# Optimization experiments

Hardware: AMD Instinct MI355X
Metric: run time of the kernel (lower is better)

## Reference

```python
import jax, jax.numpy as jnp
import numpy as np
import math

B, D, N, M = 8, 64, 4096, 4096


def setup_inputs() -> dict:
    key = jax.random.key(0)
    k1, k2, k3, k4 = jax.random.split(key, 4)
    return {
        "src_embedding": jax.random.normal(k1, (B, D, N), dtype=jnp.float32),
        "tgt_embedding": jax.random.normal(k2, (B, D, M), dtype=jnp.float32),
        "src": jax.random.normal(k3, (B, 3, N), dtype=jnp.float32),
        "tgt": jax.random.normal(k4, (B, 3, M), dtype=jnp.float32),
    }


def reference(src_embedding, tgt_embedding, src, tgt):
    d_k = src_embedding.shape[1]
    # scores: [B, N, M] = src_emb^T @ tgt_emb / sqrt(d)
    scores = jnp.einsum("bdn,bdm->bnm", src_embedding, tgt_embedding) / jnp.sqrt(
        jnp.asarray(d_k, dtype=src_embedding.dtype)
    )
    attn = jax.nn.softmax(scores, axis=2)  # softmax over target points M
    # src_corr: [B, 3, N] = tgt @ attn^T  (soft correspondence of each src point)
    src_corr = jnp.einsum("bcm,bnm->bcn", tgt, attn)
    return (src, src_corr)
```

## Files before the change

### kernel.cpp

```cpp
#include <hip/hip_runtime.h>
#include <hip/hip_bf16.h>

#define B_ 8
#define D_ 64
#define N_ 4096
#define M_ 4096
#define B3N (B_*3*N_)

#define SCALE2 0.18033688011112042f

typedef short bf16x8 __attribute__((ext_vector_type(8)));
typedef float f32x4 __attribute__((ext_vector_type(4)));
typedef __fp16 half2v __attribute__((ext_vector_type(2)));
typedef __fp16 half4v __attribute__((ext_vector_type(4)));
typedef unsigned int uint4v __attribute__((ext_vector_type(4)));

#if __has_builtin(__builtin_amdgcn_exp2f)
#define EXP2(x) __builtin_amdgcn_exp2f(x)
#else
#define EXP2(x) exp2f(x)
#endif

__device__ __forceinline__ unsigned fbits(float f) { return __builtin_bit_cast(unsigned, f); }

__device__ __forceinline__ unsigned pkbf(float hi, float lo) {
#if __has_builtin(__builtin_amdgcn_perm)
    return __builtin_amdgcn_perm(fbits(hi), fbits(lo), 0x07060302u);
#else
    return (fbits(hi) & 0xFFFF0000u) | (fbits(lo) >> 16);
#endif
}

__device__ __forceinline__ half2v pkhalf(float a, float b) {
#if __has_builtin(__builtin_amdgcn_cvt_pkrtz)
    return __builtin_bit_cast(half2v, __builtin_amdgcn_cvt_pkrtz(a, b));
#else
    half2v r; r[0] = (__fp16)a; r[1] = (__fp16)b; return r;
#endif
}

#define MFMA_PV(a,b,c) __builtin_amdgcn_mfma_f32_16x16x16f16((a),(b),(c),0,0,0)

__device__ __forceinline__ void gload_lds16(const void* g, void* lds) {
    __builtin_amdgcn_global_load_lds(
        (const __attribute__((address_space(1))) unsigned int*)g,
        (__attribute__((address_space(3))) unsigned int*)(unsigned)(unsigned long long)lds,
        16, 0, 0);
}


__global__ __launch_bounds__(64) void prep_swz_kernel(const float* __restrict__ qe,
                                                      const float* __restrict__ ke,
                                                      unsigned short* __restrict__ qs,
                                                      unsigned short* __restrict__ ks)
{
    int blk = blockIdx.x;
    bool isq = blk >= 512;
    int l  = blk & 511;
    int b  = l >> 6;
    int p  = ((l & 63) << 6) + threadIdx.x;
    const float* ip = (isq ? qe : ke) + (size_t)b * D_ * M_ + p;
    unsigned short* op = (isq ? qs : ks) + (size_t)b * M_ * D_
                       + (size_t)(p >> 4) * 1024 + (p & 15) * 8;
    float sc = isq ? SCALE2 : 1.0f;
    #pragma unroll
    for (int i = 0; i < 8; ++i) {
        float v[8];
        #pragma unroll
        for (int d = 0; d < 8; ++d) v[d] = ip[(size_t)(8*i + d) * M_] * sc;
        uint4v w;
        #pragma unroll
        for (int j = 0; j < 4; ++j) w[j] = pkbf(v[2*j+1], v[2*j]);
        *(uint4v*)(op + (i>>2)*512 + (i&3)*128) = w;
    }
}

__global__ __launch_bounds__(256) void prep3_kernel(const float4* __restrict__ src4,
                                                    const float* __restrict__ tgt,
                                                    float4* __restrict__ out4,
                                                    __fp16* __restrict__ thswz)
{
    int blk = blockIdx.x;
    if (blk < 96) {
        int i = blk*256 + threadIdx.x;
        out4[i] = src4[i];
        return;
    }
    int unit = (blk - 96)*4 + (threadIdx.x >> 6);
    int b = unit >> 8, mblk = unit & 255;
    int l = threadIdx.x & 63;
    int c = l & 3, g = l >> 4;
    int m = mblk*16 + 4*g;
    float4 tv;
    if (c < 3) tv = *(const float4*)(tgt + ((size_t)b*3 + c)*M_ + m);
    else       tv = make_float4(1.f, 1.f, 1.f, 1.f);
    half2v a01 = pkhalf(tv.x, tv.y);
    half2v a23 = pkhalf(tv.z, tv.w);
    half4v af = __builtin_shufflevector(a01, a23, 0, 1, 2, 3);
    *(half4v*)((char*)thswz + (size_t)unit*512 + l*8) = af;
}

template<int S>
__global__ __launch_bounds__(256, 4)
void attn9_kernel(const unsigned short* __restrict__ qswz,
                  const unsigned short* __restrict__ kswz,
                  const __fp16* __restrict__ thswz,
                  float* __restrict__ partials)
{
    __shared__ __align__(16) unsigned char kbuf[2][16384];

    const int lane = threadIdx.x & 63;
    const int wave = threadIdx.x >> 6;
    const int lm = lane & 15, g = lane >> 4;
    const int b = blockIdx.z, slice = blockIdx.y;
    const int n0 = blockIdx.x * 256 + wave * 64;
    const int mchunk = M_ / S, mbase = slice * mchunk;

    const char* qp = (const char*)qswz
                   + ((size_t)b * N_ * D_ + (size_t)(n0 >> 4) * 1024) * 2;
    bf16x8 qf[4][2];
    #pragma unroll
    for (int f = 0; f < 4; ++f) {
        qf[f][0] = *(const bf16x8*)(qp + f*2048 + lane*16);
        qf[f][1] = *(const bf16x8*)(qp + f*2048 + 1024 + lane*16);
    }

    const char* kp = (const char*)kswz
                   + ((size_t)b * M_ * D_ + (size_t)(mbase >> 4) * 1024) * 2
                   + lane*16;
    const char* tp = (const char*)thswz
                   + ((size_t)b * (M_/16) + (size_t)(mbase >> 4)) * 512;

    #pragma unroll
    for (int i = 0; i < 4; ++i)
        gload_lds16(kp + wave*4096 + i*1024, kbuf[0] + wave*4096 + i*1024);
    __syncthreads();

    f32x4 D2[4] = {{0,0,0,0},{0,0,0,0},{0,0,0,0},{0,0,0,0}};

    auto compute = [&](bf16x8 kA, bf16x8 kB, half4v aF) {
        #pragma unroll
        for (int f = 0; f < 4; ++f) {
            f32x4 c4 = {0,0,0,0};
            c4 = __builtin_amdgcn_mfma_f32_16x16x32_bf16(kA, qf[f][0], c4, 0, 0, 0);
            c4 = __builtin_amdgcn_mfma_f32_16x16x32_bf16(kB, qf[f][1], c4, 0, 0, 0);
            float e0 = EXP2(c4[0]);
            float e1 = EXP2(c4[1]);
            float e2 = EXP2(c4[2]);
            float e3 = EXP2(c4[3]);
            half2v p01 = pkhalf(e0, e1);
            half2v p23 = pkhalf(e2, e3);
            half4v pbf = __builtin_shufflevector(p01, p23, 0, 1, 2, 3);
            D2[f] = MFMA_PV(aF, pbf, D2[f]);
        }
    };

    int cur = 0;
    const int rounds = mchunk / 128;
    for (int r = 0; r < rounds; ++r) {
        if (r < rounds - 1) {
            const char* ksrc = kp + (r+1)*16384 + wave*4096;
            #pragma unroll
            for (int i = 0; i < 4; ++i)
                gload_lds16(ksrc + i*1024, kbuf[cur^1] + wave*4096 + i*1024);
        }
        #pragma unroll
        for (int it = 0; it < 4; ++it) {
            const unsigned char* kb4 = kbuf[cur] + it*4096;
            bf16x8 ka0 = *(const bf16x8*)(kb4 + 0*1024 + lane*16);
            bf16x8 kb0 = *(const bf16x8*)(kb4 + 1*1024 + lane*16);
            bf16x8 ka1 = *(const bf16x8*)(kb4 + 2*1024 + lane*16);
            bf16x8 kb1 = *(const bf16x8*)(kb4 + 3*1024 + lane*16);
            const char* tpi = tp + (r*4 + it)*1024;
            half4v af0 = *(const half4v*)(tpi + lane*8);
            half4v af1 = *(const half4v*)(tpi + 512 + lane*8);
            compute(ka0, kb0, af0);
            compute(ka1, kb1, af1);
        }
        __syncthreads();
        cur ^= 1;
    }

    {
        size_t base = ((size_t)slice * B_ + b) * 4 * N_ + (size_t)g * N_;
        const int sel = (g + 3) & 3;
        #pragma unroll
        for (int f = 0; f < 4; ++f)
            partials[base + n0 + 16*f + lm] = D2[f][sel];
    }
}

__global__ __launch_bounds__(64) void prep_kernel(const float* __restrict__ qe,
                                                  const float* __restrict__ ke,
                                                  unsigned short* __restrict__ qb,
                                                  unsigned short* __restrict__ kb)
{
    int blk = blockIdx.x;
    bool isq = blk >= 512;
    int l  = blk & 511;
    int b  = l >> 6;
    int p  = ((l & 63) << 6) + threadIdx.x;
    const float* ip = (isq ? qe : ke) + (size_t)b * D_ * M_ + p;
    unsigned short* op = (isq ? qb : kb) + ((size_t)b * M_ + p) * D_;
    float sc = isq ? SCALE2 : 1.0f;
    #pragma unroll
    for (int i = 0; i < 8; ++i) {
        float v[8];
        #pragma unroll
        for (int d = 0; d < 8; ++d) v[d] = ip[(size_t)(8*i + d) * M_] * sc;
        uint4v w;
        #pragma unroll
        for (int j = 0; j < 4; ++j) w[j] = pkbf(v[2*j+1], v[2*j]);
        *(uint4v*)(op + 8*i) = w;
    }
}

template<int S>
__global__ __launch_bounds__(64, 4)
void attn2_kernel(const unsigned short* __restrict__ qb,
                  const unsigned short* __restrict__ kb,
                  const float* __restrict__ tgt,
                  float* __restrict__ partials)
{
    const int t  = threadIdx.x, lm = t & 15, g = t >> 4;
    const int b  = blockIdx.z, slice = blockIdx.y, n0 = blockIdx.x * 64;
    const int mchunk = M_ / S, mbase = slice * mchunk;

    bf16x8 qf[4][2];
    #pragma unroll
    for (int f = 0; f < 4; ++f) {
        const unsigned short* qrow = qb + ((size_t)b * N_ + n0 + 16*f + lm) * D_ + 8*g;
        qf[f][0] = *(const bf16x8*)(qrow);
        qf[f][1] = *(const bf16x8*)(qrow + 32);
    }

    const bool isones = (lm & 3) == 3;
    const int  c_ld   = isones ? 2 : (lm & 3);
    half2v one2 = pkhalf(1.0f, 1.0f);
    const half4v ones4 = __builtin_shufflevector(one2, one2, 0, 1, 0, 1);

    const unsigned short* krow = kb + ((size_t)b * M_ + mbase + lm) * D_ + 8*g;
    const float* tp = tgt + ((size_t)b * 3 + c_ld) * M_ + mbase + 4*g;

    f32x4 D2[4] = {{0,0,0,0},{0,0,0,0},{0,0,0,0},{0,0,0,0}};

    for (int ms = 0; ms < mchunk; ms += 16) {
        bf16x8 ka  = *(const bf16x8*)(krow);
        bf16x8 kb8 = *(const bf16x8*)(krow + 32);
        f32x4 tv = *(const f32x4*)(tp);
        half2v a01 = pkhalf(tv[0], tv[1]);
        half2v a23 = pkhalf(tv[2], tv[3]);
        half4v afr = __builtin_shufflevector(a01, a23, 0, 1, 2, 3);
        afr = isones ? ones4 : afr;

        #pragma unroll
        for (int f = 0; f < 4; ++f) {
            f32x4 c4 = {0,0,0,0};
            c4 = __builtin_amdgcn_mfma_f32_16x16x32_bf16(ka,  qf[f][0], c4, 0, 0, 0);
            c4 = __builtin_amdgcn_mfma_f32_16x16x32_bf16(kb8, qf[f][1], c4, 0, 0, 0);
            float e0 = EXP2(c4[0]);
            float e1 = EXP2(c4[1]);
            float e2 = EXP2(c4[2]);
            float e3 = EXP2(c4[3]);
            half2v p01 = pkhalf(e0, e1);
            half2v p23 = pkhalf(e2, e3);
            half4v pbf = __builtin_shufflevector(p01, p23, 0, 1, 2, 3);
            D2[f] = MFMA_PV(afr, pbf, D2[f]);
        }
        krow += 16 * D_;
        tp   += 16;
    }

    if (t < 16) {
        size_t base = ((size_t)slice * B_ + b) * 4 * N_;
        #pragma unroll
        for (int f = 0; f < 4; ++f) {
            int n = n0 + 16*f + t;
            partials[base + 0*N_ + n] = D2[f][3];
            partials[base + 1*N_ + n] = D2[f][0];
            partials[base + 2*N_ + n] = D2[f][1];
            partials[base + 3*N_ + n] = D2[f][2];
        }
    }
}

__global__ void copy_kernel(const float4* __restrict__ src, float4* __restrict__ out) {
    int i = blockIdx.x*256 + threadIdx.x;
    out[i] = src[i];
}

template<int S>
__global__ void finalize_kernel(const float* __restrict__ ws, float* __restrict__ out) {
    int tid = blockIdx.x*256 + threadIdx.x;
    int b = tid >> 12;
    int n = tid & (N_-1);
    float den = 0.f, x = 0.f, y = 0.f, z = 0.f;
    #pragma unroll
    for (int s = 0; s < S; ++s) {
        size_t base = ((size_t)s*B_ + b)*4*N_ + n;
        den += ws[base];
        x   += ws[base + 1*N_];
        y   += ws[base + 2*N_];
        z   += ws[base + 3*N_];
    }
    float inv = 1.0f/den;
    out[B3N + ((size_t)b*3 + 0)*N_ + n] = x*inv;
    out[B3N + ((size_t)b*3 + 1)*N_ + n] = y*inv;
    out[B3N + ((size_t)b*3 + 2)*N_ + n] = z*inv;
}

extern "C" void kernel_launch(void* const* d_in, const int* in_sizes, int n_in,
                              void* d_out, int out_size, void* d_ws, size_t ws_size,
                              hipStream_t stream) {
    const float* qe  = (const float*)d_in[0];
    const float* ke  = (const float*)d_in[1];
    const float* src = (const float*)d_in[2];
    const float* tg  = (const float*)d_in[3];
    float* out = (float*)d_out;

    const size_t embElems = (size_t)B_ * M_ * D_;
    const size_t embBytes = 2 * embElems * 2;
    const size_t thBytes  = (size_t)B_ * 256 * 512;
    const size_t partB8   = (size_t)8 * B_ * 4 * N_ * 4;
    const size_t needSwz  = embBytes + thBytes + partB8;
    const size_t needOld  = embBytes + partB8;

    unsigned short* kb16 = (unsigned short*)d_ws;
    unsigned short* qb16 = kb16 + embElems;
    __fp16* thswz = (__fp16*)((char*)d_ws + embBytes);
    float* partialsNew = (float*)((char*)d_ws + embBytes + thBytes);
    float* partialsOld = (float*)((char*)d_ws + embBytes);

    if (ws_size >= needSwz) {
        prep_swz_kernel<<<1024, 64, 0, stream>>>(qe, ke, qb16, kb16);
        prep3_kernel<<<608, 256, 0, stream>>>((const float4*)src, tg, (float4*)out, thswz);
        dim3 grid(N_/256, 8, B_);
        attn9_kernel<8><<<grid, 256, 0, stream>>>(qb16, kb16, thswz, partialsNew);
        finalize_kernel<8><<<(B_*N_)/256, 256, 0, stream>>>(partialsNew, out);
    } else if (ws_size >= needOld) {
        copy_kernel<<<96, 256, 0, stream>>>((const float4*)src, (float4*)out);
        prep_kernel<<<1024, 64, 0, stream>>>(qe, ke, qb16, kb16);
        dim3 grid(N_/64, 8, B_);
        attn2_kernel<8><<<grid, 64, 0, stream>>>(qb16, kb16, tg, partialsOld);
        finalize_kernel<8><<<(B_*N_)/256, 256, 0, stream>>>(partialsOld, out);
    }
}
```

Baseline: 37.93 us.

## Merge prep kernels, stage tgt fragments via LDS, raise MFMA wave priority

Combines the two preprocessing kernels into one launch, so one kernel launch and its gap are removed. In the attention kernel, the per-iteration global loads of the swizzled target fragments move into double-buffered LDS through async global_load_lds, prefetched alongside the K tiles. The compute section is wrapped in s_setprio so MFMA-issuing waves get higher scheduling priority. This costs 8KB more LDS per block, which may reduce occupancy.

Result: faster. 34.96 us, median of 2 (-7.8%).

```diff
diff --git a/kernel.cpp b/kernel.cpp
--- a/kernel.cpp
+++ b/kernel.cpp
@@ -49,65 +49,62 @@
 }
 
 
-__global__ __launch_bounds__(64) void prep_swz_kernel(const float* __restrict__ qe,
-                                                      const float* __restrict__ ke,
-                                                      unsigned short* __restrict__ qs,
-                                                      unsigned short* __restrict__ ks)
+__global__ __launch_bounds__(256)
+void prep_all_kernel(const float* __restrict__ qe, const float* __restrict__ ke,
+                     const float4* __restrict__ src4, const float* __restrict__ tgt,
+                     unsigned short* __restrict__ qs, unsigned short* __restrict__ ks,
+                     float4* __restrict__ out4, __fp16* __restrict__ thswz)
 {
-    int blk = blockIdx.x;
-    bool isq = blk >= 512;
-    int l  = blk & 511;
-    int b  = l >> 6;
-    int p  = ((l & 63) << 6) + threadIdx.x;
-    const float* ip = (isq ? qe : ke) + (size_t)b * D_ * M_ + p;
-    unsigned short* op = (isq ? qs : ks) + (size_t)b * M_ * D_
-                       + (size_t)(p >> 4) * 1024 + (p & 15) * 8;
-    float sc = isq ? SCALE2 : 1.0f;
-    #pragma unroll
-    for (int i = 0; i < 8; ++i) {
-        float v[8];
-        #pragma unroll
-        for (int d = 0; d < 8; ++d) v[d] = ip[(size_t)(8*i + d) * M_] * sc;
-        uint4v w;
-        #pragma unroll
-        for (int j = 0; j < 4; ++j) w[j] = pkbf(v[2*j+1], v[2*j]);
-        *(uint4v*)(op + (i>>2)*512 + (i&3)*128) = w;
-    }
-}
-
-__global__ __launch_bounds__(256) void prep3_kernel(const float4* __restrict__ src4,
-                                                    const float* __restrict__ tgt,
-                                                    float4* __restrict__ out4,
-                                                    __fp16* __restrict__ thswz)
-{
-    int blk = blockIdx.x;
-    if (blk < 96) {
-        int i = blk*256 + threadIdx.x;
+    const int blk = blockIdx.x;
+    if (blk < 256) {
+        int unit = blk*4 + (threadIdx.x >> 6);
+        int t64  = threadIdx.x & 63;
+        bool isq = unit >= 512;
+        int l = unit & 511;
+        int b = l >> 6;
+        int p = ((l & 63) << 6) + t64;
+        const float* ip = (isq ? qe : ke) + (size_t)b * D_ * M_ + p;
+        unsigned short* op = (isq ? qs : ks) + (size_t)b * M_ * D_
+                           + (size_t)(p >> 4) * 1024 + (p & 15) * 8;
+        float sc = isq ? SCALE2 : 1.0f;
+        #pragma unroll
+        for (int i = 0; i < 8; ++i) {
+            float v[8];
+            #pragma unroll
+            for (int d = 0; d < 8; ++d) v[d] = ip[(size_t)(8*i + d) * M_] * sc;
+            uint4v w;
+            #pragma unroll
+            for (int j = 0; j < 4; ++j) w[j] = pkbf(v[2*j+1], v[2*j]);
+            *(uint4v*)(op + (i>>2)*512 + (i&3)*128) = w;
+        }
+    } else if (blk < 352) {
+        int i = (blk - 256)*256 + threadIdx.x;
         out4[i] = src4[i];
-        return;
-    }
-    int unit = (blk - 96)*4 + (threadIdx.x >> 6);
-    int b = unit >> 8, mblk = unit & 255;
-    int l = threadIdx.x & 63;
-    int c = l & 3, g = l >> 4;
-    int m = mblk*16 + 4*g;
-    float4 tv;
-    if (c < 3) tv = *(const float4*)(tgt + ((size_t)b*3 + c)*M_ + m);
-    else       tv = make_float4(1.f, 1.f, 1.f, 1.f);
-    half2v a01 = pkhalf(tv.x, tv.y);
-    half2v a23 = pkhalf(tv.z, tv.w);
-    half4v af = __builtin_shufflevector(a01, a23, 0, 1, 2, 3);
-    *(half4v*)((char*)thswz + (size_t)unit*512 + l*8) = af;
+    } else {
+        int unit = (blk - 352)*4 + (threadIdx.x >> 6);
+        int b = unit >> 8, mblk = unit & 255;
+        int l = threadIdx.x & 63;
+        int c = l & 3, g = l >> 4;
+        int m = mblk*16 + 4*g;
+        float4 tv;
+        if (c < 3) tv = *(const float4*)(tgt + ((size_t)b*3 + c)*M_ + m);
+        else       tv = make_float4(1.f, 1.f, 1.f, 1.f);
+        half2v a01 = pkhalf(tv.x, tv.y);
+        half2v a23 = pkhalf(tv.z, tv.w);
+        half4v af = __builtin_shufflevector(a01, a23, 0, 1, 2, 3);
+        *(half4v*)((char*)thswz + (size_t)unit*512 + l*8) = af;
+    }
 }
 
 template<int S>
 __global__ __launch_bounds__(256, 4)
-void attn9_kernel(const unsigned short* __restrict__ qswz,
-                  const unsigned short* __restrict__ kswz,
-                  const __fp16* __restrict__ thswz,
-                  float* __restrict__ partials)
+void attn10_kernel(const unsigned short* __restrict__ qswz,
+                   const unsigned short* __restrict__ kswz,
+                   const __fp16* __restrict__ thswz,
+                   float* __restrict__ partials)
 {
     __shared__ __align__(16) unsigned char kbuf[2][16384];
+    __shared__ __align__(16) unsigned char abuf[2][4096];
 
     const int lane = threadIdx.x & 63;
     const int wave = threadIdx.x >> 6;
@@ -129,11 +126,13 @@
                    + ((size_t)b * M_ * D_ + (size_t)(mbase >> 4) * 1024) * 2
                    + lane*16;
     const char* tp = (const char*)thswz
-                   + ((size_t)b * (M_/16) + (size_t)(mbase >> 4)) * 512;
+                   + ((size_t)b * (M_/16) + (size_t)(mbase >> 4)) * 512
+                   + lane*16;
 
     #pragma unroll
     for (int i = 0; i < 4; ++i)
         gload_lds16(kp + wave*4096 + i*1024, kbuf[0] + wave*4096 + i*1024);
+    gload_lds16(tp + wave*1024, abuf[0] + wave*1024);
     __syncthreads();
 
     f32x4 D2[4] = {{0,0,0,0},{0,0,0,0},{0,0,0,0},{0,0,0,0}};
@@ -163,6 +162,7 @@
             #pragma unroll
             for (int i = 0; i < 4; ++i)
                 gload_lds16(ksrc + i*1024, kbuf[cur^1] + wave*4096 + i*1024);
+            gload_lds16(tp + (r+1)*4096 + wave*1024, abuf[cur^1] + wave*1024);
         }
         #pragma unroll
         for (int it = 0; it < 4; ++it) {
@@ -171,11 +171,13 @@
             bf16x8 kb0 = *(const bf16x8*)(kb4 + 1*1024 + lane*16);
             bf16x8 ka1 = *(const bf16x8*)(kb4 + 2*1024 + lane*16);
             bf16x8 kb1 = *(const bf16x8*)(kb4 + 3*1024 + lane*16);
-            const char* tpi = tp + (r*4 + it)*1024;
-            half4v af0 = *(const half4v*)(tpi + lane*8);
-            half4v af1 = *(const half4v*)(tpi + 512 + lane*8);
+            const unsigned char* ab = abuf[cur] + it*1024;
+            half4v af0 = *(const half4v*)(ab + lane*8);
+            half4v af1 = *(const half4v*)(ab + 512 + lane*8);
+            __builtin_amdgcn_s_setprio(1);
             compute(ka0, kb0, af0);
             compute(ka1, kb1, af1);
+            __builtin_amdgcn_s_setprio(0);
         }
         __syncthreads();
         cur ^= 1;
@@ -332,10 +334,10 @@
     float* partialsOld = (float*)((char*)d_ws + embBytes);
 
     if (ws_size >= needSwz) {
-        prep_swz_kernel<<<1024, 64, 0, stream>>>(qe, ke, qb16, kb16);
-        prep3_kernel<<<608, 256, 0, stream>>>((const float4*)src, tg, (float4*)out, thswz);
+        prep_all_kernel<<<864, 256, 0, stream>>>(qe, ke, (const float4*)src, tg,
+                                                 qb16, kb16, (float4*)out, thswz);
         dim3 grid(N_/256, 8, B_);
-        attn9_kernel<8><<<grid, 256, 0, stream>>>(qb16, kb16, thswz, partialsNew);
+        attn10_kernel<8><<<grid, 256, 0, stream>>>(qb16, kb16, thswz, partialsNew);
         finalize_kernel<8><<<(B_*N_)/256, 256, 0, stream>>>(partialsNew, out);
     } else if (ws_size >= needOld) {
         copy_kernel<<<96, 256, 0, stream>>>((const float4*)src, (float4*)out);
```
